# Kernel tuning notes

Hardware: AMD Instinct MI355X
Metric: run time of the kernel (lower is better)

The kernel has to match this reference:

```python
import jax, jax.numpy as jnp
import numpy as np

ALPHA, GAMMA, THRESHOLD, NUM_CLASSES = 0.5, 1.5, 0.5, 21
EPS8, EPS7 = 1e-8, 1e-7


def corner_to_center(b):
    w = b[..., 2] - b[..., 0]
    h = b[..., 3] - b[..., 1]
    cx = b[..., 0] + w / 2
    cy = b[..., 1] + h / 2
    return jnp.stack([cx, cy, w, h], axis=-1)


def box_iou(b1, b2):
    # b1: [P,4], b2: [M,4] -> [P,M]
    area1 = (b1[:, 2] - b1[:, 0]) * (b1[:, 3] - b1[:, 1])
    area2 = (b2[:, 2] - b2[:, 0]) * (b2[:, 3] - b2[:, 1])
    lt = jnp.maximum(b1[:, None, :2], b2[None, :, :2])
    rb = jnp.minimum(b1[:, None, 2:], b2[None, :, 2:])
    wh = jnp.clip(rb - lt, 0)
    inter = wh[..., 0] * wh[..., 1]
    return inter / (area1[:, None] + area2[None, :] - inter)


def encode_boxes(matched, dbox):
    g = corner_to_center(matched)
    d = corner_to_center(dbox)
    ex = (g[..., 0] - d[..., 0]) / (d[..., 2] + EPS8)
    ey = (g[..., 1] - d[..., 1]) / (d[..., 3] + EPS8)
    ew = jnp.log(g[..., 2] / (d[..., 2] + EPS8) + EPS8)
    eh = jnp.log(g[..., 3] / (d[..., 3] + EPS8) + EPS8)
    return jnp.stack([ex, ey, ew, eh], axis=-1)


def decode_boxes(loc, dbox):
    d = corner_to_center(dbox)
    cx = loc[..., 0] * d[..., 2] + d[..., 0]
    cy = loc[..., 1] * d[..., 3] + d[..., 1]
    w = jnp.exp(loc[..., 2]) * d[..., 2]
    h = jnp.exp(loc[..., 3]) * d[..., 3]
    return jnp.stack([cx - w / 2, cy - h / 2, cx + w / 2, cy + h / 2], axis=-1)


def giou_loss(pred, tgt):
    inter_min = jnp.maximum(pred[..., :2], tgt[..., :2])
    inter_max = jnp.minimum(pred[..., 2:], tgt[..., 2:])
    inter_wh = jnp.clip(inter_max - inter_min, 0)
    inter = inter_wh[..., 0] * inter_wh[..., 1]
    pa = (pred[..., 2] - pred[..., 0]) * (pred[..., 3] - pred[..., 1])
    ta = (tgt[..., 2] - tgt[..., 0]) * (tgt[..., 3] - tgt[..., 1])
    union = pa + ta - inter
    iou = inter / (union + EPS7)
    encl_min = jnp.minimum(pred[..., :2], tgt[..., :2])
    encl_max = jnp.maximum(pred[..., 2:], tgt[..., 2:])
    encl_wh = jnp.clip(encl_max - encl_min, 0)
    encl = encl_wh[..., 0] * encl_wh[..., 1]
    giou = iou - (encl - union) / (encl + EPS7)
    return 1.0 - giou


def _match_one(truths, labels, dbox):
    # truths: [M,4], labels: [M], dbox: [P,4]
    M = truths.shape[0]
    overlaps = box_iou(dbox, truths)               # [P,M]
    bt_ov = overlaps.max(axis=1)                   # [P]
    bt_idx = overlaps.argmax(axis=1)               # [P]
    bp_idx = overlaps.argmax(axis=0)               # [M] best prior per GT
    # force-match each GT to its best prior
    bt_idx = bt_idx.at[bp_idx].set(jnp.arange(M))
    bt_ov = bt_ov.at[bp_idx].set(2.0)
    matches = truths[bt_idx]                       # [P,4]
    mlabels = jnp.where(bt_ov < THRESHOLD, 0, labels[bt_idx])
    loc_t = encode_boxes(matches, dbox)
    return loc_t, mlabels


def focal_loss(pred, target):
    # pred: [N,C], target: [N]
    logp = jax.nn.log_softmax(pred, axis=-1)
    ce = -jnp.take_along_axis(logp, target[:, None], axis=1)[:, 0]
    p_t = jnp.exp(-ce)
    return ALPHA * (1.0 - p_t) ** GAMMA * ce


def setup_inputs() -> dict:
    key = jax.random.key(0)
    k1, k2, k3, k4, k5, k6, k7 = jax.random.split(key, 7)
    B, P, M, C = 64, 24564, 50, 21
    # valid corner-format boxes: min + positive wh
    d_min = jax.random.uniform(k1, (P, 2)) * 0.8
    d_wh = 0.05 + jax.random.uniform(k2, (P, 2)) * 0.2
    default_boxes = jnp.concatenate([d_min, d_min + d_wh], axis=1)
    g_min = jax.random.uniform(k3, (B, M, 2)) * 0.8
    g_wh = 0.05 + jax.random.uniform(k4, (B, M, 2)) * 0.2
    gt_boxes = jnp.concatenate([g_min, g_min + g_wh], axis=2)
    loc_preds = jax.random.normal(k5, (B, P, 4)) * 0.1
    conf_preds = jax.random.normal(k6, (B, P, C))
    gt_labels = jax.random.randint(k7, (B, M), 1, C)
    return {"loc_preds": loc_preds, "conf_preds": conf_preds,
            "default_boxes": default_boxes, "gt_boxes": gt_boxes,
            "gt_labels": gt_labels}


def reference(loc_preds, conf_preds, default_boxes, gt_boxes, gt_labels):
    B, P, _ = loc_preds.shape
    loc_t, conf_t = jax.vmap(_match_one, in_axes=(0, 0, None))(gt_boxes, gt_labels, default_boxes)
    pos = conf_t > 0                                   # [B,P]
    num_pos = pos.sum()
    denom = jnp.maximum(num_pos, 1).astype(loc_preds.dtype)
    # localization: decode preds and targets against anchors, GIoU on positives
    decoded_pred = decode_boxes(loc_preds, default_boxes[None])
    decoded_tgt = decode_boxes(loc_t, default_boxes[None])
    gl = giou_loss(decoded_pred, decoded_tgt)          # [B,P]
    loc_loss = jnp.sum(jnp.where(pos, gl, 0.0)) / denom
    # classification: focal loss over all anchors
    fl = focal_loss(conf_preds.reshape(-1, conf_preds.shape[-1]), conf_t.reshape(-1))
    conf_loss = fl.sum() / denom
    total = loc_loss + conf_loss
    return jnp.where(num_pos == 0, 0.0, total)
```

## Files before the change

### kernel.cpp

```cpp
#include <hip/hip_runtime.h>
#include <cstdint>
#include <cstddef>

#define F_ALPHA 0.5f
#define THRESH  0.5f
#define EPS8    1e-8f
#define EPS7    1e-7f
#define MAXM    64
#define CCLS    21
#define GGRP    4

__global__ __launch_bounds__(256)
void bp_kernel(const float4* __restrict__ dbox,
               const float4* __restrict__ gt,
               unsigned* __restrict__ bp,
               int P, int M)
{
    __shared__ unsigned long long wkey[GGRP][4];

    const int b  = blockIdx.y;
    const int m0 = blockIdx.x * GGRP;
    const int t  = threadIdx.x;
    const int w  = t >> 6, lane = t & 63;

    float4 gb[GGRP]; float ga[GGRP];
    #pragma unroll
    for (int g = 0; g < GGRP; g++) {
        int m = min(m0 + g, M - 1);
        float4 gg = gt[(size_t)b * M + m];
        gb[g] = gg;
        ga[g] = (gg.z - gg.x) * (gg.w - gg.y);
    }

    float    bestv[GGRP];
    unsigned bestp[GGRP];
    #pragma unroll
    for (int g = 0; g < GGRP; g++) { bestv[g] = 0.f; bestp[g] = 0u; }

    for (int p = t; p < P; p += 256) {
        float4 d = dbox[p];
        float darea = (d.z - d.x) * (d.w - d.y);
        #pragma unroll
        for (int g = 0; g < GGRP; g++) {
            float4 gg = gb[g];
            float lx = fmaxf(d.x, gg.x), ly = fmaxf(d.y, gg.y);
            float rx = fminf(d.z, gg.z), ry = fminf(d.w, gg.w);
            float iw = fmaxf(rx - lx, 0.f), ih = fmaxf(ry - ly, 0.f);
            float inter = iw * ih;
            float iou = inter * __builtin_amdgcn_rcpf(darea + ga[g] - inter);
            if (iou > bestv[g]) { bestv[g] = iou; bestp[g] = (unsigned)p; }
        }
    }

    #pragma unroll
    for (int g = 0; g < GGRP; g++) {
        unsigned long long k =
            ((unsigned long long)__float_as_uint(bestv[g]) << 32)
            | (unsigned long long)(0xFFFFFFFFu - bestp[g]);
        #pragma unroll
        for (int o = 1; o < 64; o <<= 1) {
            unsigned long long k2 = __shfl_xor(k, o, 64);
            if (k2 > k) k = k2;
        }
        if (lane == 0) wkey[g][w] = k;
    }
    __syncthreads();
    if (t < GGRP) {
        unsigned long long k0 = wkey[t][0], k1 = wkey[t][1];
        unsigned long long k2 = wkey[t][2], k3 = wkey[t][3];
        unsigned long long ka = (k0 > k1) ? k0 : k1;
        unsigned long long kb = (k2 > k3) ? k2 : k3;
        unsigned long long k  = (ka > kb) ? ka : kb;
        int m = m0 + t;
        if (m < M)
            bp[(size_t)b * M + m] = 0xFFFFFFFFu - (unsigned)(k & 0xFFFFFFFFull);
    }
}

__global__ __launch_bounds__(256)
void loss_kernel(const float4* __restrict__ locp,
                 const float*  __restrict__ conf,
                 const float4* __restrict__ dbox,
                 const float4* __restrict__ gt,
                 const int*    __restrict__ gtl,
                 const unsigned* __restrict__ bp,
                 double* __restrict__ partS,
                 int*    __restrict__ partC,
                 int P, int M)
{
    __shared__ float    scf[256 * CCLS];
    __shared__ float4   tb[MAXM];
    __shared__ float    tarea[MAXM];
    __shared__ int      tl[MAXM];
    __shared__ unsigned bpp[MAXM];
    __shared__ double   sv[4];
    __shared__ int      sc[4];

    const int t = threadIdx.x;
    const int b = blockIdx.y;
    const int p0 = blockIdx.x * 256;
    const int p = p0 + t;

    if (t < M) {
        float4 g = gt[(size_t)b * M + t];
        tb[t] = g;
        tarea[t] = (g.z - g.x) * (g.w - g.y);
        tl[t] = gtl[(size_t)b * M + t];
        bpp[t] = bp[(size_t)b * M + t];
    }

    const int cnt = min(256, P - p0);
    const int nf = cnt * CCLS;
    const float* src = conf + ((size_t)b * P + p0) * CCLS;
    if (((uintptr_t)src & 15) == 0) {
        const int n4 = nf >> 2;
        const float4* s4 = (const float4*)src;
        float4* d4 = (float4*)scf;
        for (int i = t; i < n4; i += 256) d4[i] = s4[i];
        for (int i = (n4 << 2) + t; i < nf; i += 256) scf[i] = src[i];
    } else {
        for (int i = t; i < nf; i += 256) scf[i] = src[i];
    }
    __syncthreads();

    double acc = 0.0;
    int cnt_pos = 0;
    if (p < P) {
        float4 d = dbox[p];
        const float dw_ = d.z - d.x, dh_ = d.w - d.y;
        const float darea = dw_ * dh_;

        float best = -1.0f;
        int   bm = 0;
        for (int m = 0; m < M; m++) {
            float4 g = tb[m];
            float lx = fmaxf(d.x, g.x), ly = fmaxf(d.y, g.y);
            float rx = fminf(d.z, g.z), ry = fminf(d.w, g.w);
            float iw = fmaxf(rx - lx, 0.f), ih = fmaxf(ry - ly, 0.f);
            float inter = iw * ih;
            float iou = inter * __builtin_amdgcn_rcpf(darea + tarea[m] - inter);
            if (iou > best) { best = iou; bm = m; }
        }

        int  idx = bm;
        bool pos = (best >= THRESH);
        for (int j = 0; j < M; j++) {
            if (bpp[j] == (unsigned)p) { idx = j; pos = true; }
        }
        int lbl = pos ? tl[idx] : 0;

        const float* x = scf + t * CCLS;
        float mx = -1e30f;
        #pragma unroll
        for (int c = 0; c < CCLS; c++) mx = fmaxf(mx, x[c]);
        float sum = 0.f;
        #pragma unroll
        for (int c = 0; c < CCLS; c++) sum += expf(x[c] - mx);
        float ce = (mx + logf(sum)) - x[lbl];
        float pt = expf(-ce);
        float om = 1.f - pt;
        acc = (double)(F_ALPHA * om * sqrtf(om) * ce);

        if (pos) {
            cnt_pos = 1;
            float dw = dw_, dh = dh_;
            float dcx = d.x + dw * 0.5f, dcy = d.y + dh * 0.5f;
            float4 g = tb[idx];
            float gw = g.z - g.x, gh = g.w - g.y;
            float gcx = g.x + gw * 0.5f, gcy = g.y + gh * 0.5f;
            float ex = (gcx - dcx) / (dw + EPS8);
            float ey = (gcy - dcy) / (dh + EPS8);
            float ew = logf(gw / (dw + EPS8) + EPS8);
            float eh = logf(gh / (dh + EPS8) + EPS8);
            float tcx = ex * dw + dcx, tcy = ey * dh + dcy;
            float tw = expf(ew) * dw,  th = expf(eh) * dh;
            float t0 = tcx - tw * 0.5f, t1 = tcy - th * 0.5f;
            float t2 = tcx + tw * 0.5f, t3 = tcy + th * 0.5f;
            float4 l = locp[(size_t)b * P + p];
            float pcx = l.x * dw + dcx, pcy = l.y * dh + dcy;
            float pw = expf(l.z) * dw,  ph = expf(l.w) * dh;
            float q0 = pcx - pw * 0.5f, q1 = pcy - ph * 0.5f;
            float q2 = pcx + pw * 0.5f, q3 = pcy + ph * 0.5f;
            float ix0 = fmaxf(q0, t0), iy0 = fmaxf(q1, t1);
            float ix1 = fminf(q2, t2), iy1 = fminf(q3, t3);
            float iw = fmaxf(ix1 - ix0, 0.f), ih = fmaxf(iy1 - iy0, 0.f);
            float inter = iw * ih;
            float pa = (q2 - q0) * (q3 - q1);
            float ta = (t2 - t0) * (t3 - t1);
            float uni = pa + ta - inter;
            float iou = inter / (uni + EPS7);
            float e0 = fminf(q0, t0), e1 = fminf(q1, t1);
            float e2 = fmaxf(q2, t2), e3 = fmaxf(q3, t3);
            float ewd = fmaxf(e2 - e0, 0.f), ehd = fmaxf(e3 - e1, 0.f);
            float encl = ewd * ehd;
            float giou = iou - (encl - uni) / (encl + EPS7);
            acc += (double)(1.f - giou);
        }
    }

    for (int o = 32; o > 0; o >>= 1) {
        acc += __shfl_down(acc, o, 64);
        cnt_pos += __shfl_down(cnt_pos, o, 64);
    }
    int w = t >> 6, lane = t & 63;
    if (lane == 0) { sv[w] = acc; sc[w] = cnt_pos; }
    __syncthreads();
    if (t == 0) {
        int slot = blockIdx.y * gridDim.x + blockIdx.x;
        partS[slot] = sv[0] + sv[1] + sv[2] + sv[3];
        partC[slot] = sc[0] + sc[1] + sc[2] + sc[3];
    }
}

__global__ __launch_bounds__(256)
void final_kernel(const double* __restrict__ partS,
                  const int*    __restrict__ partC,
                  float* __restrict__ out, int n)
{
    __shared__ double sv[4];
    __shared__ long long sc[4];
    const int t = threadIdx.x;
    double a = 0.0; long long c = 0;
    for (int i = t; i < n; i += 256) { a += partS[i]; c += partC[i]; }
    for (int o = 32; o > 0; o >>= 1) {
        a += __shfl_down(a, o, 64);
        c += __shfl_down(c, o, 64);
    }
    int w = t >> 6, lane = t & 63;
    if (lane == 0) { sv[w] = a; sc[w] = c; }
    __syncthreads();
    if (t == 0) {
        double s = sv[0] + sv[1] + sv[2] + sv[3];
        long long np = sc[0] + sc[1] + sc[2] + sc[3];
        out[0] = (np == 0) ? 0.0f : (float)(s / (double)np);
    }
}

extern "C" void kernel_launch(void* const* d_in, const int* in_sizes, int n_in,
                              void* d_out, int out_size, void* d_ws, size_t ws_size,
                              hipStream_t stream)
{
    const float* locp = (const float*)d_in[0];
    const float* conf = (const float*)d_in[1];
    const float* dbox = (const float*)d_in[2];
    const float* gt   = (const float*)d_in[3];
    const int*   gtl  = (const int*)d_in[4];

    const int P  = in_sizes[2] / 4;
    const long long BP = (long long)in_sizes[0] / 4;
    const int B  = (int)(BP / P);
    const int M  = in_sizes[4] / B;

    const int nblk = (P + 255) / 256;
    const int nPart = nblk * B;

    char* ws = (char*)d_ws;
    unsigned* bp = (unsigned*)ws;
    size_t off = ((size_t)B * M * 4 + 15) & ~(size_t)15;
    double* partS = (double*)(ws + off);
    off += (size_t)nPart * 8;
    int* partC = (int*)(ws + off);

    dim3 gridBP((M + GGRP - 1) / GGRP, B);
    dim3 grid(nblk, B);
    bp_kernel<<<gridBP, 256, 0, stream>>>((const float4*)dbox, (const float4*)gt,
                                          bp, P, M);
    loss_kernel<<<grid, 256, 0, stream>>>((const float4*)locp, conf,
                                          (const float4*)dbox, (const float4*)gt,
                                          gtl, bp, partS, partC, P, M);
    final_kernel<<<1, 256, 0, stream>>>(partS, partC, (float*)d_out, nPart);
}
```

Before: 301.2 us.

## Restructure anchor matching: global GT reads, division-free IoU compare, shared override map

Matching now reads GT boxes and areas (precomputed in bp_kernel) from global memory with uniform addresses, instead of from LDS. The IoU argmax compares cross-multiplied fractions, which removes the reciprocal per pair. The per-anchor scan over all best-prior indices is replaced by a shared override table filled with atomicMax. Other changes: the class logits are loaded into registers, the float4 copy no longer checks alignment, and the launch bounds request 6 waves per SIMD. Risks: the cross-multiply compare can tie-break differently from the reference's float division, and dropping the alignment check assumes the conf rows are 16-byte aligned.

```diff
diff --git a/kernel.cpp b/kernel.cpp
--- a/kernel.cpp
+++ b/kernel.cpp
@@ -14,6 +14,7 @@
 void bp_kernel(const float4* __restrict__ dbox,
                const float4* __restrict__ gt,
                unsigned* __restrict__ bp,
+               float* __restrict__ garea,
                int P, int M)
 {
     __shared__ unsigned long long wkey[GGRP][4];
@@ -72,16 +73,20 @@
         unsigned long long kb = (k2 > k3) ? k2 : k3;
         unsigned long long k  = (ka > kb) ? ka : kb;
         int m = m0 + t;
-        if (m < M)
+        if (m < M) {
             bp[(size_t)b * M + m] = 0xFFFFFFFFu - (unsigned)(k & 0xFFFFFFFFull);
-    }
-}
-
-__global__ __launch_bounds__(256)
+            float4 gg = gt[(size_t)b * M + m];
+            garea[(size_t)b * M + m] = (gg.z - gg.x) * (gg.w - gg.y);
+        }
+    }
+}
+
+__global__ __launch_bounds__(256, 6)
 void loss_kernel(const float4* __restrict__ locp,
                  const float*  __restrict__ conf,
                  const float4* __restrict__ dbox,
                  const float4* __restrict__ gt,
+                 const float*  __restrict__ garea,
                  const int*    __restrict__ gtl,
                  const unsigned* __restrict__ bp,
                  double* __restrict__ partS,
@@ -90,9 +95,8 @@
 {
     __shared__ float    scf[256 * CCLS];
     __shared__ float4   tb[MAXM];
-    __shared__ float    tarea[MAXM];
     __shared__ int      tl[MAXM];
-    __shared__ unsigned bpp[MAXM];
+    __shared__ int      ovr[256];
     __shared__ double   sv[4];
     __shared__ int      sc[4];
 
@@ -100,70 +104,85 @@
     const int b = blockIdx.y;
     const int p0 = blockIdx.x * 256;
     const int p = p0 + t;
-
+    const bool valid = (p < P);
+
+    ovr[t] = -1;
     if (t < M) {
-        float4 g = gt[(size_t)b * M + t];
-        tb[t] = g;
-        tarea[t] = (g.z - g.x) * (g.w - g.y);
+        tb[t] = gt[(size_t)b * M + t];
         tl[t] = gtl[(size_t)b * M + t];
-        bpp[t] = bp[(size_t)b * M + t];
     }
 
     const int cnt = min(256, P - p0);
     const int nf = cnt * CCLS;
     const float* src = conf + ((size_t)b * P + p0) * CCLS;
-    if (((uintptr_t)src & 15) == 0) {
+    {
         const int n4 = nf >> 2;
         const float4* s4 = (const float4*)src;
         float4* d4 = (float4*)scf;
         for (int i = t; i < n4; i += 256) d4[i] = s4[i];
         for (int i = (n4 << 2) + t; i < nf; i += 256) scf[i] = src[i];
-    } else {
-        for (int i = t; i < nf; i += 256) scf[i] = src[i];
+    }
+    __syncthreads();
+
+    if (t < M) {
+        unsigned q = bp[(size_t)b * M + t] - (unsigned)p0;
+        if (q < 256u) atomicMax(&ovr[q], t);
+    }
+
+    float4 d = make_float4(0.f, 0.f, 0.f, 0.f);
+    float bi = -1.0f, bd = 1.0f;
+    int   bm = 0;
+    if (valid) {
+        d = dbox[p];
+        const float darea = (d.z - d.x) * (d.w - d.y);
+        const float4* gtb = gt + (size_t)b * M;
+        const float*  gab = garea + (size_t)b * M;
+        const int Mpad = (M + 3) & ~3;
+        for (int m0 = 0; m0 < Mpad; m0 += 4) {
+            #pragma unroll
+            for (int k = 0; k < 4; k++) {
+                int mc = min(m0 + k, M - 1);
+                float4 g = gtb[mc];
+                float ta = gab[mc];
+                float lx = fmaxf(d.x, g.x), ly = fmaxf(d.y, g.y);
+                float rx = fminf(d.z, g.z), ry = fminf(d.w, g.w);
+                float iw = fmaxf(rx - lx, 0.f), ih = fmaxf(ry - ly, 0.f);
+                float inter = iw * ih;
+                float den = darea + ta - inter;
+                if (inter * bd > bi * den) { bi = inter; bd = den; bm = m0 + k; }
+            }
+        }
     }
     __syncthreads();
 
     double acc = 0.0;
     int cnt_pos = 0;
-    if (p < P) {
-        float4 d = dbox[p];
-        const float dw_ = d.z - d.x, dh_ = d.w - d.y;
-        const float darea = dw_ * dh_;
-
-        float best = -1.0f;
-        int   bm = 0;
-        for (int m = 0; m < M; m++) {
-            float4 g = tb[m];
-            float lx = fmaxf(d.x, g.x), ly = fmaxf(d.y, g.y);
-            float rx = fminf(d.z, g.z), ry = fminf(d.w, g.w);
-            float iw = fmaxf(rx - lx, 0.f), ih = fmaxf(ry - ly, 0.f);
-            float inter = iw * ih;
-            float iou = inter * __builtin_amdgcn_rcpf(darea + tarea[m] - inter);
-            if (iou > best) { best = iou; bm = m; }
-        }
-
+    if (valid) {
         int  idx = bm;
-        bool pos = (best >= THRESH);
-        for (int j = 0; j < M; j++) {
-            if (bpp[j] == (unsigned)p) { idx = j; pos = true; }
-        }
+        bool pos = (bi >= THRESH * bd);
+        int j = ovr[t];
+        if (j >= 0) { idx = j; pos = true; }
         int lbl = pos ? tl[idx] : 0;
 
+        float xv[CCLS];
         const float* x = scf + t * CCLS;
-        float mx = -1e30f;
-        #pragma unroll
-        for (int c = 0; c < CCLS; c++) mx = fmaxf(mx, x[c]);
+        #pragma unroll
+        for (int c = 0; c < CCLS; c++) xv[c] = x[c];
+        float xl = scf[t * CCLS + lbl];
+        float mx = xv[0];
+        #pragma unroll
+        for (int c = 1; c < CCLS; c++) mx = fmaxf(mx, xv[c]);
         float sum = 0.f;
         #pragma unroll
-        for (int c = 0; c < CCLS; c++) sum += expf(x[c] - mx);
-        float ce = (mx + logf(sum)) - x[lbl];
+        for (int c = 0; c < CCLS; c++) sum += expf(xv[c] - mx);
+        float ce = (mx + logf(sum)) - xl;
         float pt = expf(-ce);
         float om = 1.f - pt;
         acc = (double)(F_ALPHA * om * sqrtf(om) * ce);
 
         if (pos) {
             cnt_pos = 1;
-            float dw = dw_, dh = dh_;
+            float dw = d.z - d.x, dh = d.w - d.y;
             float dcx = d.x + dw * 0.5f, dcy = d.y + dh * 0.5f;
             float4 g = tb[idx];
             float gw = g.z - g.x, gh = g.w - g.y;
@@ -257,6 +276,8 @@
     char* ws = (char*)d_ws;
     unsigned* bp = (unsigned*)ws;
     size_t off = ((size_t)B * M * 4 + 15) & ~(size_t)15;
+    float* garea = (float*)(ws + off);
+    off += ((size_t)B * M * 4 + 15) & ~(size_t)15;
     double* partS = (double*)(ws + off);
     off += (size_t)nPart * 8;
     int* partC = (int*)(ws + off);
@@ -264,9 +285,9 @@
     dim3 gridBP((M + GGRP - 1) / GGRP, B);
     dim3 grid(nblk, B);
     bp_kernel<<<gridBP, 256, 0, stream>>>((const float4*)dbox, (const float4*)gt,
-                                          bp, P, M);
+                                          bp, garea, P, M);
     loss_kernel<<<grid, 256, 0, stream>>>((const float4*)locp, conf,
                                           (const float4*)dbox, (const float4*)gt,
-                                          gtl, bp, partS, partC, P, M);
+                                          garea, gtl, bp, partS, partC, P, M);
     final_kernel<<<1, 256, 0, stream>>>(partS, partC, (float*)d_out, nPart);
 }
```

After: 302.2 us. No clear change (+0.3%).
